# Kernel tuning notes

Measured on AMD Instinct MI355X. Metric: run time of the kernel, lower is better.

The kernel has to match this reference:

```python
import jax, jax.numpy as jnp
import numpy as np
from jax import lax

S, B, C = 7, 2, 20
W, H = 448.0, 448.0
IOU_THR = 0.1
PROB_THR = 8e-25
BATCH = 16
L = S * S * C + S * S * B + S * S * B * 4  # 1470
N = S * S * B * C                          # 1960 (box,class) candidates per image


def setup_inputs() -> dict:
    key = jax.random.key(0)
    prediction = jax.random.uniform(key, (BATCH, L), dtype=jnp.float32)
    return {"prediction": prediction}


def _pairwise_iou(b):
    # b: [N,4] boxes as (x_center, y_center, w, h); faithful to YoloDetector.iou
    x, y, w, h = b[:, 0], b[:, 1], b[:, 2], b[:, 3]
    tb = (jnp.minimum(x[:, None] + 0.5 * w[:, None], x[None, :] + 0.5 * w[None, :])
          - jnp.maximum(x[:, None] - 0.5 * w[:, None], x[None, :] - 0.5 * w[None, :]))
    lr = (jnp.minimum(y[:, None] + 0.5 * h[:, None], y[None, :] + 0.5 * h[None, :])
          - jnp.maximum(y[:, None] - 0.5 * h[:, None], y[None, :] - 0.5 * h[None, :]))
    inter = jnp.where((tb < 0) | (lr < 0), 0.0, tb * lr)
    area = w * h
    return inter / (area[:, None] + area[None, :] - inter)


def _decode_one(pred):
    # split flat prediction as in traDim(mode=3)
    SC, SB = S * S * C, S * S * B
    class_prob = pred[:SC].reshape(S, S, C)
    confidence = pred[SC:SC + SB].reshape(S, S, B)
    boxes = pred[SC + SB:].reshape(S, S, B, 4)

    # grid offsets: boxes[...,0] += row index i, boxes[...,1] += col index j
    idx = jnp.arange(S, dtype=pred.dtype)
    x = (boxes[..., 0] + idx[:, None, None]) / S * W
    y = (boxes[..., 1] + idx[None, :, None]) / S * H
    w = boxes[..., 2] * boxes[..., 2] * W
    h = boxes[..., 3] * boxes[..., 3] * H
    boxes_xywh = jnp.stack([x, y, w, h], axis=-1)          # [S,S,B,4]

    # eProbs[i,j,b,c] = classProb[i,j,c] * confidence[i,j,b]
    e_probs = class_prob[:, :, None, :] * confidence[:, :, :, None]  # [S,S,B,C]
    mask = e_probs >= PROB_THR
    # original uses argmax over the boolean mask along class axis for the class id
    cls = jnp.argmax(mask, axis=3)                         # [S,S,B]

    # flatten all (cell, box, class) candidates; below-threshold probs -> 0 (masking
    # replaces the data-dependent boolean filtering of the original)
    probs = jnp.where(mask, e_probs, 0.0).reshape(-1)                          # [N]
    boxes_c = jnp.broadcast_to(boxes_xywh[:, :, :, None, :], (S, S, B, C, 4)).reshape(-1, 4)
    cls_c = jnp.broadcast_to(cls[:, :, :, None], (S, S, B, C)).reshape(-1)     # [N]

    order = jnp.argsort(-probs)                            # descending by prob
    probs = probs[order]
    boxes_c = boxes_c[order]
    cls_c = cls_c[order]

    iou = _pairwise_iou(boxes_c)                           # [N,N], memory-dominant

    def step(p, xs):
        row, i = xs
        pivot = p[i]
        sup = (jnp.arange(N) > i) & (row > IOU_THR) & (pivot > 0)
        return jnp.where(sup, 0.0, p), None

    probs_nms, _ = lax.scan(step, probs, (iou, jnp.arange(N)))
    return boxes_c, probs_nms, cls_c


def reference(prediction):
    # returns (boxes [BATCH,N,4], probs_after_nms [BATCH,N], class_ids [BATCH,N]);
    # suppressed / sub-threshold candidates carry prob == 0 (fixed-shape analogue of
    # the original's boolean filtering)
    return jax.vmap(_decode_one)(prediction)
```

## Files before the change

### kernel.cpp

```cpp
#include <hip/hip_runtime.h>


constexpr int S_  = 7;
constexpr int Cc  = 20;
constexpr int NBOX  = 98;
constexpr int NENT  = 1960;
constexpr int NPAD  = 2048;
constexpr int LPRED = 1470;
constexpr int BATCH = 16;
constexpr float IOU_THR_  = 0.1f;
constexpr float PROB_THR_ = 8e-25f;

__global__ __launch_bounds__(1024)
void yolo_nms_kernel(const float* __restrict__ pred_all, float* __restrict__ out)
{
    const int b   = blockIdx.x;
    const int tid = threadIdx.x;
    const float* pred = pred_all + b * LPRED;

    __shared__ float s_pred[LPRED];
    __shared__ unsigned long long s_k[NPAD];
    __shared__ float bXh[NBOX], bXl[NBOX], bYh[NBOX], bYl[NBOX], bA[NBOX];
    __shared__ float4 bBox[NBOX];
    __shared__ unsigned int clsMask[NBOX];
    __shared__ unsigned long long iouRow[NBOX * 2];
    __shared__ int firstpos[NBOX];
    __shared__ int boxorder[NBOX];
    __shared__ int kept[NBOX];
    __shared__ int s_nvalid;

    for (int i = tid; i < LPRED; i += 1024) s_pred[i] = pred[i];
    if (tid == 0) s_nvalid = 0;
    if (tid < NBOX) { clsMask[tid] = 0u; kept[tid] = 0; firstpos[tid] = 0x7FFFFFFF; }
    if (tid < 2 * NBOX) iouRow[tid] = 0ull;
    __syncthreads();

    if (tid < NBOX) {
        const int bo = tid, cell = bo >> 1;
        const int ci = cell / S_, cj = cell % S_;
        const float bx = s_pred[1078 + bo * 4 + 0];
        const float by = s_pred[1078 + bo * 4 + 1];
        const float bw = s_pred[1078 + bo * 4 + 2];
        const float bh = s_pred[1078 + bo * 4 + 3];
        const float x = (bx + (float)ci) / 7.0f * 448.0f;
        const float y = (by + (float)cj) / 7.0f * 448.0f;
        const float w = bw * bw * 448.0f;
        const float h = bh * bh * 448.0f;
        bBox[bo] = make_float4(x, y, w, h);
        bXh[bo] = x + 0.5f * w;  bXl[bo] = x - 0.5f * w;
        bYh[bo] = y + 0.5f * h;  bYl[bo] = y - 0.5f * h;
        bA[bo]  = w * h;
    }
    __syncthreads();

    for (int e = tid; e < NPAD; e += 1024) {
        unsigned long long key = 0ull;
        if (e < NENT) {
            const int bo = e / Cc, c = e - bo * Cc, cell = bo >> 1;
            const float ep = s_pred[cell * Cc + c] * s_pred[980 + bo];
            if (ep >= PROB_THR_) {
                atomicOr(&clsMask[bo], 1u << c);
                key = ((unsigned long long)__float_as_uint(ep) << 32)
                    | (unsigned long long)(0xFFFFFFFFu - (unsigned)e);
            } else {
                key = (unsigned long long)(0xFFFFFFFFu - (unsigned)e);
            }
        }
        s_k[e] = key;
    }
    for (int t = tid; t < NBOX * NBOX; t += 1024) {
        const int i = t / NBOX, j = t - i * NBOX;
        const float tb = fminf(bXh[i], bXh[j]) - fmaxf(bXl[i], bXl[j]);
        const float lr = fminf(bYh[i], bYh[j]) - fmaxf(bYl[i], bYl[j]);
        const float inter = (tb < 0.0f || lr < 0.0f) ? 0.0f : tb * lr;
        const float iou = inter / (bA[i] + bA[j] - inter);
        if (iou > IOU_THR_) atomicOr(&iouRow[i * 2 + (j >> 6)], 1ull << (j & 63));
    }
    __syncthreads();

    for (int k = 2; k <= NPAD; k <<= 1) {
        for (int js = k >> 1; js > 0; js >>= 1) {
            const int idx = ((tid & ~(js - 1)) << 1) | (tid & (js - 1));
            const int l   = idx | js;
            const unsigned long long a = s_k[idx], c = s_k[l];
            const bool dir = ((idx & k) == 0);
            if ((a < c) == dir) { s_k[idx] = c; s_k[l] = a; }
            __syncthreads();
        }
    }

    for (int kp = tid; kp < NENT; kp += 1024) {
        const unsigned long long key = s_k[kp];
        if ((key >> 32) != 0ull) {
            const int idx = (int)(0xFFFFFFFFu - (unsigned)key);
            atomicMin(&firstpos[idx / Cc], kp);
        }
    }
    __syncthreads();

    if (tid < NBOX) {
        const int fp = firstpos[tid];
        if (fp != 0x7FFFFFFF) {
            int r = 0;
            for (int b2 = 0; b2 < NBOX; ++b2) r += (firstpos[b2] < fp) ? 1 : 0;
            boxorder[r] = tid;
            atomicAdd(&s_nvalid, 1);
        }
    }
    __syncthreads();

    if (tid == 0) {
        unsigned long long sup0 = 0ull, sup1 = 0ull;
        const int nv = s_nvalid;
        for (int r = 0; r < nv; ++r) {
            const int bb = boxorder[r];
            const unsigned long long r0 = iouRow[bb * 2];
            const unsigned long long r1 = iouRow[bb * 2 + 1];
            const bool supd = (bb < 64) ? ((sup0 >> bb) & 1ull)
                                        : ((sup1 >> (bb - 64)) & 1ull);
            if (!supd) { kept[bb] = 1; sup0 |= r0; sup1 |= r1; }
        }
    }
    __syncthreads();

    float* outBoxes = out + b * (NENT * 4);
    float* outProbs = out + BATCH * NENT * 4 + b * NENT;
    float* outCls   = out + BATCH * NENT * 5 + b * NENT;
    for (int kp = tid; kp < NENT; kp += 1024) {
        const unsigned long long key = s_k[kp];
        const unsigned pb = (unsigned)(key >> 32);
        const int idx = (int)(0xFFFFFFFFu - (unsigned)key);
        const int bo  = idx / Cc;
        *reinterpret_cast<float4*>(outBoxes + kp * 4) = bBox[bo];
        outProbs[kp] = (pb != 0u && kp == firstpos[bo] && kept[bo])
                         ? __uint_as_float(pb) : 0.0f;
        const unsigned cm = clsMask[bo];
        outCls[kp] = (float)(cm ? (__ffs(cm) - 1) : 0);
    }
}

extern "C" void kernel_launch(void* const* d_in, const int* in_sizes, int n_in,
                              void* d_out, int out_size, void* d_ws, size_t ws_size,
                              hipStream_t stream)
{
    const float* pred = (const float*)d_in[0];
    float* out = (float*)d_out;
    yolo_nms_kernel<<<BATCH, 1024, 0, stream>>>(pred, out);
}
```

Baseline: 34.20 us.

## Register-resident bitonic sort with wave shuffles, ballot-based IoU masks

The bitonic sort now keeps two keys per thread in registers. Stages with stride under 64 use wave shuffles, the 1024 stride is an in-register swap, and only the middle strides go through double-buffered shared memory with one barrier each. This removes most of the block-wide barriers and the shared-memory traffic of the original sort. The IoU bitmask is built per row by one wave with __ballot instead of shared atomicOr, and the class id comes from a per-box scan instead of atomic masks. The trade-off is extra register pressure and more complex indexing.

```diff
diff --git a/kernel.cpp b/kernel.cpp
--- a/kernel.cpp
+++ b/kernel.cpp
@@ -11,18 +11,30 @@
 constexpr float IOU_THR_  = 0.1f;
 constexpr float PROB_THR_ = 8e-25f;
 
+__device__ __forceinline__ unsigned long long
+cmpsel(unsigned long long mine, unsigned long long part, int idx, int js, int k)
+{
+    const bool desc  = ((idx & k) == 0);
+    const bool lower = ((idx & js) == 0);
+    const bool keep_max = (lower == desc);
+    const unsigned long long mx = mine > part ? mine : part;
+    const unsigned long long mn = mine > part ? part : mine;
+    return keep_max ? mx : mn;
+}
+
 __global__ __launch_bounds__(1024)
 void yolo_nms_kernel(const float* __restrict__ pred_all, float* __restrict__ out)
 {
     const int b   = blockIdx.x;
     const int tid = threadIdx.x;
+    const int wid = tid >> 6, lane = tid & 63;
     const float* pred = pred_all + b * LPRED;
 
     __shared__ float s_pred[LPRED];
-    __shared__ unsigned long long s_k[NPAD];
+    __shared__ unsigned long long s_buf[2][NPAD];
     __shared__ float bXh[NBOX], bXl[NBOX], bYh[NBOX], bYl[NBOX], bA[NBOX];
     __shared__ float4 bBox[NBOX];
-    __shared__ unsigned int clsMask[NBOX];
+    __shared__ int   bCls[NBOX];
     __shared__ unsigned long long iouRow[NBOX * 2];
     __shared__ int firstpos[NBOX];
     __shared__ int boxorder[NBOX];
@@ -31,8 +43,7 @@
 
     for (int i = tid; i < LPRED; i += 1024) s_pred[i] = pred[i];
     if (tid == 0) s_nvalid = 0;
-    if (tid < NBOX) { clsMask[tid] = 0u; kept[tid] = 0; firstpos[tid] = 0x7FFFFFFF; }
-    if (tid < 2 * NBOX) iouRow[tid] = 0ull;
+    if (tid < NBOX) { kept[tid] = 0; firstpos[tid] = 0x7FFFFFFF; }
     __syncthreads();
 
     if (tid < NBOX) {
@@ -50,52 +61,86 @@
         bXh[bo] = x + 0.5f * w;  bXl[bo] = x - 0.5f * w;
         bYh[bo] = y + 0.5f * h;  bYl[bo] = y - 0.5f * h;
         bA[bo]  = w * h;
+        const float conf = s_pred[980 + bo];
+        int cls = 0;
+        for (int c = 0; c < Cc; ++c)
+            if (s_pred[cell * Cc + c] * conf >= PROB_THR_) { cls = c; break; }
+        bCls[bo] = cls;
     }
+
+    auto makekey = [&](int e) -> unsigned long long {
+        if (e >= NENT) return 0ull;
+        const int bo = e / Cc, c = e - bo * Cc, cell = bo >> 1;
+        const float ep = s_pred[cell * Cc + c] * s_pred[980 + bo];
+        unsigned long long key = (unsigned long long)(0xFFFFFFFFu - (unsigned)e);
+        if (ep >= PROB_THR_)
+            key |= ((unsigned long long)__float_as_uint(ep) << 32);
+        return key;
+    };
     __syncthreads();
+    unsigned long long A  = makekey(tid);
+    unsigned long long Bv = makekey(tid + 1024);
 
-    for (int e = tid; e < NPAD; e += 1024) {
-        unsigned long long key = 0ull;
-        if (e < NENT) {
-            const int bo = e / Cc, c = e - bo * Cc, cell = bo >> 1;
-            const float ep = s_pred[cell * Cc + c] * s_pred[980 + bo];
-            if (ep >= PROB_THR_) {
-                atomicOr(&clsMask[bo], 1u << c);
-                key = ((unsigned long long)__float_as_uint(ep) << 32)
-                    | (unsigned long long)(0xFFFFFFFFu - (unsigned)e);
-            } else {
-                key = (unsigned long long)(0xFFFFFFFFu - (unsigned)e);
+    for (int r = wid; r < NBOX; r += 16) {
+        const float rXh = bXh[r], rXl = bXl[r], rYh = bYh[r], rYl = bYl[r], rA = bA[r];
+        bool s1 = false, s2 = false;
+        {
+            const int j = lane;
+            if (j < NBOX) {
+                const float tb = fminf(rXh, bXh[j]) - fmaxf(rXl, bXl[j]);
+                const float lr = fminf(rYh, bYh[j]) - fmaxf(rYl, bYl[j]);
+                const float inter = (tb < 0.0f || lr < 0.0f) ? 0.0f : tb * lr;
+                const float iou = inter / (rA + bA[j] - inter);
+                s1 = (iou > IOU_THR_);
             }
         }
-        s_k[e] = key;
+        {
+            const int j = lane + 64;
+            if (j < NBOX) {
+                const float tb = fminf(rXh, bXh[j]) - fmaxf(rXl, bXl[j]);
+                const float lr = fminf(rYh, bYh[j]) - fmaxf(rYl, bYl[j]);
+                const float inter = (tb < 0.0f || lr < 0.0f) ? 0.0f : tb * lr;
+                const float iou = inter / (rA + bA[j] - inter);
+                s2 = (iou > IOU_THR_);
+            }
+        }
+        const unsigned long long m1 = __ballot(s1);
+        const unsigned long long m2 = __ballot(s2);
+        if (lane == 0) { iouRow[r * 2] = m1; iouRow[r * 2 + 1] = m2; }
     }
-    for (int t = tid; t < NBOX * NBOX; t += 1024) {
-        const int i = t / NBOX, j = t - i * NBOX;
-        const float tb = fminf(bXh[i], bXh[j]) - fmaxf(bXl[i], bXl[j]);
-        const float lr = fminf(bYh[i], bYh[j]) - fmaxf(bYl[i], bYl[j]);
-        const float inter = (tb < 0.0f || lr < 0.0f) ? 0.0f : tb * lr;
-        const float iou = inter / (bA[i] + bA[j] - inter);
-        if (iou > IOU_THR_) atomicOr(&iouRow[i * 2 + (j >> 6)], 1ull << (j & 63));
-    }
-    __syncthreads();
 
+    int pbuf = 0;
     for (int k = 2; k <= NPAD; k <<= 1) {
         for (int js = k >> 1; js > 0; js >>= 1) {
-            const int idx = ((tid & ~(js - 1)) << 1) | (tid & (js - 1));
-            const int l   = idx | js;
-            const unsigned long long a = s_k[idx], c = s_k[l];
-            const bool dir = ((idx & k) == 0);
-            if ((a < c) == dir) { s_k[idx] = c; s_k[l] = a; }
-            __syncthreads();
+            if (js == 1024) {
+                const unsigned long long mx = A > Bv ? A : Bv;
+                const unsigned long long mn = A > Bv ? Bv : A;
+                A = mx; Bv = mn;
+            } else if (js >= 64) {
+                s_buf[pbuf][tid]        = A;
+                s_buf[pbuf][tid + 1024] = Bv;
+                __syncthreads();
+                const unsigned long long pA = s_buf[pbuf][tid ^ js];
+                const unsigned long long pB = s_buf[pbuf][(tid + 1024) ^ js];
+                A  = cmpsel(A,  pA, tid,        js, k);
+                Bv = cmpsel(Bv, pB, tid + 1024, js, k);
+                pbuf ^= 1;
+            } else {
+                const unsigned long long pA = __shfl_xor(A,  js);
+                const unsigned long long pB = __shfl_xor(Bv, js);
+                A  = cmpsel(A,  pA, tid,        js, k);
+                Bv = cmpsel(Bv, pB, tid + 1024, js, k);
+            }
         }
     }
 
-    for (int kp = tid; kp < NENT; kp += 1024) {
-        const unsigned long long key = s_k[kp];
-        if ((key >> 32) != 0ull) {
-            const int idx = (int)(0xFFFFFFFFu - (unsigned)key);
-            atomicMin(&firstpos[idx / Cc], kp);
-        }
-    }
+    unsigned long long* s_k = s_buf[0];
+    s_k[tid]        = A;
+    s_k[tid + 1024] = Bv;
+    if (A >> 32)
+        atomicMin(&firstpos[(int)(0xFFFFFFFFu - (unsigned)A) / Cc], tid);
+    if (Bv >> 32)
+        atomicMin(&firstpos[(int)(0xFFFFFFFFu - (unsigned)Bv) / Cc], tid + 1024);
     __syncthreads();
 
     if (tid < NBOX) {
@@ -128,14 +173,13 @@
     float* outCls   = out + BATCH * NENT * 5 + b * NENT;
     for (int kp = tid; kp < NENT; kp += 1024) {
         const unsigned long long key = s_k[kp];
-        const unsigned pb = (unsigned)(key >> 32);
+        const unsigned pb2 = (unsigned)(key >> 32);
         const int idx = (int)(0xFFFFFFFFu - (unsigned)key);
         const int bo  = idx / Cc;
         *reinterpret_cast<float4*>(outBoxes + kp * 4) = bBox[bo];
-        outProbs[kp] = (pb != 0u && kp == firstpos[bo] && kept[bo])
-                         ? __uint_as_float(pb) : 0.0f;
-        const unsigned cm = clsMask[bo];
-        outCls[kp] = (float)(cm ? (__ffs(cm) - 1) : 0);
+        outProbs[kp] = (pb2 != 0u && kp == firstpos[bo] && kept[bo])
+                         ? __uint_as_float(pb2) : 0.0f;
+        outCls[kp] = (float)bCls[bo];
     }
 }
 
```

Measured after the change: 38.23 us. 1.12x slower.

## Use wavefront ballots, intra-wave bitonic stages and lane-parallel NMS to cut block syncs

Applied to the files above, without the earlier changes.

The bitonic sort now skips block-wide barriers for stages whose compare distance stays inside one 64-lane wavefront, relying on an LDS wait counter instead. The IoU bitmask is built with per-row wavefront ballots rather than per-pair shared atomics, and the class id is found with a direct per-box scan instead of an atomic class mask. The serial NMS loop now runs on one wavefront, broadcasting box ids and IoU rows with readlane instead of single-thread LDS reads. Together these aim to remove barrier and atomic overhead in a latency-bound single-block-per-image kernel, at the cost of depending on wavefront-lockstep assumptions.

```diff
diff --git a/kernel.cpp b/kernel.cpp
--- a/kernel.cpp
+++ b/kernel.cpp
@@ -11,18 +11,26 @@
 constexpr float IOU_THR_  = 0.1f;
 constexpr float PROB_THR_ = 8e-25f;
 
+__device__ __forceinline__ unsigned long long rl64(unsigned long long v, int l)
+{
+    unsigned lo = (unsigned)__builtin_amdgcn_readlane((int)(unsigned)v, l);
+    unsigned hi = (unsigned)__builtin_amdgcn_readlane((int)(unsigned)(v >> 32), l);
+    return ((unsigned long long)hi << 32) | lo;
+}
+
 __global__ __launch_bounds__(1024)
 void yolo_nms_kernel(const float* __restrict__ pred_all, float* __restrict__ out)
 {
-    const int b   = blockIdx.x;
-    const int tid = threadIdx.x;
+    const int b    = blockIdx.x;
+    const int tid  = threadIdx.x;
+    const int wid  = tid >> 6, lane = tid & 63;
     const float* pred = pred_all + b * LPRED;
 
     __shared__ float s_pred[LPRED];
     __shared__ unsigned long long s_k[NPAD];
     __shared__ float bXh[NBOX], bXl[NBOX], bYh[NBOX], bYl[NBOX], bA[NBOX];
     __shared__ float4 bBox[NBOX];
-    __shared__ unsigned int clsMask[NBOX];
+    __shared__ int   bCls[NBOX];
     __shared__ unsigned long long iouRow[NBOX * 2];
     __shared__ int firstpos[NBOX];
     __shared__ int boxorder[NBOX];
@@ -31,8 +39,7 @@
 
     for (int i = tid; i < LPRED; i += 1024) s_pred[i] = pred[i];
     if (tid == 0) s_nvalid = 0;
-    if (tid < NBOX) { clsMask[tid] = 0u; kept[tid] = 0; firstpos[tid] = 0x7FFFFFFF; }
-    if (tid < 2 * NBOX) iouRow[tid] = 0ull;
+    if (tid < NBOX) { kept[tid] = 0; firstpos[tid] = 0x7FFFFFFF; }
     __syncthreads();
 
     if (tid < NBOX) {
@@ -50,51 +57,68 @@
         bXh[bo] = x + 0.5f * w;  bXl[bo] = x - 0.5f * w;
         bYh[bo] = y + 0.5f * h;  bYl[bo] = y - 0.5f * h;
         bA[bo]  = w * h;
+        const float conf = s_pred[980 + bo];
+        int cls = 0;
+        for (int c = 0; c < Cc; ++c)
+            if (s_pred[cell * Cc + c] * conf >= PROB_THR_) { cls = c; break; }
+        bCls[bo] = cls;
     }
-    __syncthreads();
 
     for (int e = tid; e < NPAD; e += 1024) {
         unsigned long long key = 0ull;
         if (e < NENT) {
             const int bo = e / Cc, c = e - bo * Cc, cell = bo >> 1;
             const float ep = s_pred[cell * Cc + c] * s_pred[980 + bo];
-            if (ep >= PROB_THR_) {
-                atomicOr(&clsMask[bo], 1u << c);
-                key = ((unsigned long long)__float_as_uint(ep) << 32)
-                    | (unsigned long long)(0xFFFFFFFFu - (unsigned)e);
-            } else {
-                key = (unsigned long long)(0xFFFFFFFFu - (unsigned)e);
-            }
+            key = (unsigned long long)(0xFFFFFFFFu - (unsigned)e);
+            if (ep >= PROB_THR_)
+                key |= ((unsigned long long)__float_as_uint(ep) << 32);
         }
         s_k[e] = key;
     }
-    for (int t = tid; t < NBOX * NBOX; t += 1024) {
-        const int i = t / NBOX, j = t - i * NBOX;
-        const float tb = fminf(bXh[i], bXh[j]) - fmaxf(bXl[i], bXl[j]);
-        const float lr = fminf(bYh[i], bYh[j]) - fmaxf(bYl[i], bYl[j]);
-        const float inter = (tb < 0.0f || lr < 0.0f) ? 0.0f : tb * lr;
-        const float iou = inter / (bA[i] + bA[j] - inter);
-        if (iou > IOU_THR_) atomicOr(&iouRow[i * 2 + (j >> 6)], 1ull << (j & 63));
+    __syncthreads();
+
+    for (int r = wid; r < NBOX; r += 16) {
+        const float rXh = bXh[r], rXl = bXl[r], rYh = bYh[r], rYl = bYl[r], rA = bA[r];
+        bool s1 = false, s2 = false;
+        {
+            const int j = lane;
+            const float tb = fminf(rXh, bXh[j]) - fmaxf(rXl, bXl[j]);
+            const float lr = fminf(rYh, bYh[j]) - fmaxf(rYl, bYl[j]);
+            const float inter = (tb < 0.0f || lr < 0.0f) ? 0.0f : tb * lr;
+            const float iou = inter / (rA + bA[j] - inter);
+            s1 = (iou > IOU_THR_);
+        }
+        if (lane + 64 < NBOX) {
+            const int j = lane + 64;
+            const float tb = fminf(rXh, bXh[j]) - fmaxf(rXl, bXl[j]);
+            const float lr = fminf(rYh, bYh[j]) - fmaxf(rYl, bYl[j]);
+            const float inter = (tb < 0.0f || lr < 0.0f) ? 0.0f : tb * lr;
+            const float iou = inter / (rA + bA[j] - inter);
+            s2 = (iou > IOU_THR_);
+        }
+        const unsigned long long m1 = __ballot(s1);
+        const unsigned long long m2 = __ballot(s2);
+        if (lane == 0) { iouRow[r * 2] = m1; iouRow[r * 2 + 1] = m2; }
     }
-    __syncthreads();
 
     for (int k = 2; k <= NPAD; k <<= 1) {
         for (int js = k >> 1; js > 0; js >>= 1) {
+            if (js >= 128) __syncthreads();
             const int idx = ((tid & ~(js - 1)) << 1) | (tid & (js - 1));
             const int l   = idx | js;
             const unsigned long long a = s_k[idx], c = s_k[l];
             const bool dir = ((idx & k) == 0);
             if ((a < c) == dir) { s_k[idx] = c; s_k[l] = a; }
-            __syncthreads();
+            if (js == 128) __syncthreads();
+            else if (js < 128) asm volatile("s_waitcnt lgkmcnt(0)" ::: "memory");
         }
     }
+    __syncthreads();
 
     for (int kp = tid; kp < NENT; kp += 1024) {
         const unsigned long long key = s_k[kp];
-        if ((key >> 32) != 0ull) {
-            const int idx = (int)(0xFFFFFFFFu - (unsigned)key);
-            atomicMin(&firstpos[idx / Cc], kp);
-        }
+        if (key >> 32)
+            atomicMin(&firstpos[(int)(0xFFFFFFFFu - (unsigned)key) / Cc], kp);
     }
     __syncthreads();
 
@@ -109,17 +133,37 @@
     }
     __syncthreads();
 
-    if (tid == 0) {
-        unsigned long long sup0 = 0ull, sup1 = 0ull;
+    if (tid < 64) {
         const int nv = s_nvalid;
+        int bb0 = -1, bb1 = -1;
+        unsigned long long r00 = 0, r01 = 0, r10 = 0, r11 = 0;
+        if (tid < nv) {
+            bb0 = boxorder[tid];
+            r00 = iouRow[bb0 * 2]; r01 = iouRow[bb0 * 2 + 1];
+        }
+        if (tid + 64 < nv) {
+            bb1 = boxorder[tid + 64];
+            r10 = iouRow[bb1 * 2]; r11 = iouRow[bb1 * 2 + 1];
+        }
+        unsigned long long sup0 = 0, sup1 = 0, k0 = 0, k1 = 0;
         for (int r = 0; r < nv; ++r) {
-            const int bb = boxorder[r];
-            const unsigned long long r0 = iouRow[bb * 2];
-            const unsigned long long r1 = iouRow[bb * 2 + 1];
-            const bool supd = (bb < 64) ? ((sup0 >> bb) & 1ull)
-                                        : ((sup1 >> (bb - 64)) & 1ull);
-            if (!supd) { kept[bb] = 1; sup0 |= r0; sup1 |= r1; }
+            int bb; unsigned long long rw0, rw1;
+            if (r < 64) {
+                bb  = __builtin_amdgcn_readlane(bb0, r);
+                rw0 = rl64(r00, r); rw1 = rl64(r01, r);
+            } else {
+                bb  = __builtin_amdgcn_readlane(bb1, r - 64);
+                rw0 = rl64(r10, r - 64); rw1 = rl64(r11, r - 64);
+            }
+            const bool supped = (bb < 64) ? ((sup0 >> bb) & 1ull)
+                                          : ((sup1 >> (bb - 64)) & 1ull);
+            if (!supped) {
+                if (bb < 64) k0 |= 1ull << bb; else k1 |= 1ull << (bb - 64);
+                sup0 |= rw0; sup1 |= rw1;
+            }
         }
+        kept[tid] = (int)((k0 >> tid) & 1ull);
+        if (tid < NBOX - 64) kept[tid + 64] = (int)((k1 >> tid) & 1ull);
     }
     __syncthreads();
 
@@ -128,14 +172,13 @@
     float* outCls   = out + BATCH * NENT * 5 + b * NENT;
     for (int kp = tid; kp < NENT; kp += 1024) {
         const unsigned long long key = s_k[kp];
-        const unsigned pb = (unsigned)(key >> 32);
+        const unsigned pb2 = (unsigned)(key >> 32);
         const int idx = (int)(0xFFFFFFFFu - (unsigned)key);
         const int bo  = idx / Cc;
         *reinterpret_cast<float4*>(outBoxes + kp * 4) = bBox[bo];
-        outProbs[kp] = (pb != 0u && kp == firstpos[bo] && kept[bo])
-                         ? __uint_as_float(pb) : 0.0f;
-        const unsigned cm = clsMask[bo];
-        outCls[kp] = (float)(cm ? (__ffs(cm) - 1) : 0);
+        outProbs[kp] = (pb2 != 0u && kp == firstpos[bo] && kept[bo])
+                         ? __uint_as_float(pb2) : 0.0f;
+        outCls[kp] = (float)bCls[bo];
     }
 }
 
```

Result: slower. 36.08 us (+5.5%).
